# Performance work log

Hardware: AMD Instinct MI355X
Metric: run time of the kernel (lower is better)

## Reference

```python
import jax, jax.numpy as jnp
import numpy as np

NUM_HEADS = 8
NUM_LAYERS = 4
BASE_THR = 0.5     # AdaptiveLIF base_threshold (state reset -> no adaptation on single step)
TAU_MEM = 5.0      # tau_mem (single step from zero state: mem = decay*0 + x = x)
SURR_SLOPE = 5.0   # fast-sigmoid surrogate slope (forward path unaffected)
EPS = 1e-5
NEG = -1e9


@jax.custom_vjp
def spike(u):
    return (u > 0.0).astype(u.dtype)

def _spike_fwd(u):
    return (u > 0.0).astype(u.dtype), u

def _spike_bwd(u, g):
    return (g / (1.0 + SURR_SLOPE * jnp.abs(u)) ** 2,)

spike.defvjp(_spike_fwd, _spike_bwd)


def lif(x):
    # AdaptiveLIF, single timestep from reset state: mem = x, thr = base_threshold
    return spike(x - BASE_THR)


def layer_norm(x, g, b):
    m = jnp.mean(x, axis=-1, keepdims=True)
    v = jnp.mean((x - m) ** 2, axis=-1, keepdims=True)
    return (x - m) * jax.lax.rsqrt(v + EPS) * g + b


def dsa(x, wq, bq, wk, bk, wv, bv, wo, bo, top_k):
    # Dynamic Sparse Attention: dense scores -> per-query top-k mask -> softmax -> AV
    B, T, D = x.shape
    H = NUM_HEADS
    dh = D // H

    def heads(w, bias):
        return (x @ w.T + bias).reshape(B, T, H, dh).transpose(0, 2, 1, 3)  # [B,H,T,dh]

    q, k, v = heads(wq, bq), heads(wk, bk), heads(wv, bv)
    scores = jnp.einsum('bhqd,bhkd->bhqk', q, k) / jnp.sqrt(jnp.asarray(dh, x.dtype))
    vals, idx = jax.lax.top_k(scores, top_k)  # [B,H,T,K]

    # scatter top-k values into a -inf-filled score matrix (exact top-k sparsity)
    N = B * H * T
    rows = jnp.arange(N)[:, None]
    sp = jnp.full((N, T), NEG, scores.dtype).at[rows, idx.reshape(N, top_k)].set(vals.reshape(N, top_k))
    attn = jax.nn.softmax(sp.reshape(B, H, T, T), axis=-1)

    out = jnp.einsum('bhqk,bhkd->bhqd', attn, v)
    out = out.transpose(0, 2, 1, 3).reshape(B, T, D)
    out = out @ wo.T + bo
    return lif(out)  # spiking output of attention


def ffn(x, w1, b1, w2, b2):
    h = lif(x @ w1.T + b1)
    return lif(h @ w2.T + b2)


def setup_inputs() -> dict:
    key = jax.random.key(0)
    ks = jax.random.split(key, 16)
    L, D, F, IN, OUT, B, T = NUM_LAYERS, 512, 2048, 128, 256, 2, 2048
    s = 0.02
    return {
        'x': jax.random.normal(ks[0], (B, T, IN), jnp.float32),
        'emb_w': jax.random.normal(ks[1], (D, IN), jnp.float32) * s,
        'emb_b': jnp.zeros((D,), jnp.float32),
        'pos_emb': jax.random.normal(ks[2], (1, T, D), jnp.float32) * s,
        'wq': jax.random.normal(ks[3], (L, D, D), jnp.float32) * s,
        'bq': jnp.zeros((L, D), jnp.float32),
        'wk': jax.random.normal(ks[4], (L, D, D), jnp.float32) * s,
        'bk': jnp.zeros((L, D), jnp.float32),
        'wv': jax.random.normal(ks[5], (L, D, D), jnp.float32) * s,
        'bv': jnp.zeros((L, D), jnp.float32),
        'wo': jax.random.normal(ks[6], (L, D, D), jnp.float32) * s,
        'bo': jnp.zeros((L, D), jnp.float32),
        'ln1_g': jnp.ones((L, D), jnp.float32),
        'ln1_b': jnp.zeros((L, D), jnp.float32),
        'fc1_w': jax.random.normal(ks[7], (L, F, D), jnp.float32) * s,
        'fc1_b': jnp.zeros((L, F), jnp.float32),
        'fc2_w': jax.random.normal(ks[8], (L, D, F), jnp.float32) * s,
        'fc2_b': jnp.zeros((L, D), jnp.float32),
        'ln2_g': jnp.ones((L, D), jnp.float32),
        'ln2_b': jnp.zeros((L, D), jnp.float32),
        'fnorm_g': jnp.ones((D,), jnp.float32),
        'fnorm_b': jnp.zeros((D,), jnp.float32),
        'cls_w': jax.random.normal(ks[9], (OUT, D), jnp.float32) * s,
        'cls_b': jnp.zeros((OUT,), jnp.float32),
        'top_k': 32,
    }


def reference(x, emb_w, emb_b, pos_emb, wq, bq, wk, bk, wv, bv, wo, bo,
              ln1_g, ln1_b, fc1_w, fc1_b, fc2_w, fc2_b, ln2_g, ln2_b,
              fnorm_g, fnorm_b, cls_w, cls_b, top_k):
    B, T, _ = x.shape
    h = x @ emb_w.T + emb_b + pos_emb[:, :T, :]
    for l in range(NUM_LAYERS):
        a = dsa(h, wq[l], bq[l], wk[l], bk[l], wv[l], bv[l], wo[l], bo[l], top_k)
        h = layer_norm(h + a, ln1_g[l], ln1_b[l])
        f = ffn(h, fc1_w[l], fc1_b[l], fc2_w[l], fc2_b[l])
        h = layer_norm(h + f, ln2_g[l], ln2_b[l])
    h = layer_norm(h, fnorm_g, fnorm_b)
    pooled = jnp.mean(h, axis=1)  # [B, D]
    return pooled @ cls_w.T + cls_b
```

## Files before the change

kernel.cpp:

```cpp
#include <hip/hip_runtime.h>
#include <math.h>
#include <float.h>

#define T_SEQ  2048
#define DMODEL 512
#define NHEAD  8
#define DHEAD  64
#define FDIM   2048
#define NLAYER 4
#define NB     2
#define MROWS  (NB*T_SEQ)

typedef _Float16 f16x8 __attribute__((ext_vector_type(8)));
typedef float    f32x4 __attribute__((ext_vector_type(4)));

__device__ __forceinline__ void async16(const _Float16* g, _Float16* l) {
    __builtin_amdgcn_global_load_lds(
        (const __attribute__((address_space(1))) unsigned int*)g,
        (__attribute__((address_space(3))) unsigned int*)l, 16, 0, 0);
}

template<int BN, int EPI>
__global__ __launch_bounds__(256) void gemm_k(
    const float* __restrict__ A, const float* __restrict__ W,
    const float* __restrict__ bias, const float* __restrict__ pos,
    float* __restrict__ C, int M, int N, int K)
{
    constexpr int BM = 128;
    constexpr int BK = 32;
    constexpr int MN = BN / 16;
    __shared__ float As[BK][BM + 4];
    __shared__ float Ws[BK][BN + 4];
    const int tid = threadIdx.x;
    const int n0 = blockIdx.x * BN;
    const int m0 = blockIdx.y * BM;
    const int tx = tid & 15;
    const int ty = tid >> 4;

    float acc[8][MN];
    #pragma unroll
    for (int i = 0; i < 8; ++i)
        #pragma unroll
        for (int j = 0; j < MN; ++j) acc[i][j] = 0.f;

    for (int k0 = 0; k0 < K; k0 += BK) {
        #pragma unroll
        for (int it = 0; it < 4; ++it) {
            int qq = tid + 256 * it;
            int m = qq >> 3, kq = qq & 7;
            float4 v4 = *(const float4*)(A + (size_t)(m0 + m) * K + k0 + kq * 4);
            As[kq*4+0][m] = v4.x; As[kq*4+1][m] = v4.y;
            As[kq*4+2][m] = v4.z; As[kq*4+3][m] = v4.w;
        }
        #pragma unroll
        for (int it = 0; it < BN/32; ++it) {
            int qq = tid + 256 * it;
            int n = qq >> 3, kq = qq & 7;
            float4 v4 = *(const float4*)(W + (size_t)(n0 + n) * K + k0 + kq * 4);
            Ws[kq*4+0][n] = v4.x; Ws[kq*4+1][n] = v4.y;
            Ws[kq*4+2][n] = v4.z; Ws[kq*4+3][n] = v4.w;
        }
        __syncthreads();
        for (int kk = 0; kk < BK; ++kk) {
            float a[8], b[MN];
            float4 a0 = *(const float4*)&As[kk][ty*8];
            float4 a1 = *(const float4*)&As[kk][ty*8+4];
            a[0]=a0.x; a[1]=a0.y; a[2]=a0.z; a[3]=a0.w;
            a[4]=a1.x; a[5]=a1.y; a[6]=a1.z; a[7]=a1.w;
            float4 b0 = *(const float4*)&Ws[kk][tx*4];
            b[0]=b0.x; b[1]=b0.y; b[2]=b0.z; b[3]=b0.w;
            if constexpr (MN == 8) {
                float4 b1 = *(const float4*)&Ws[kk][64 + tx*4];
                b[4]=b1.x; b[5]=b1.y; b[6]=b1.z; b[7]=b1.w;
            }
            #pragma unroll
            for (int i = 0; i < 8; ++i)
                #pragma unroll
                for (int j = 0; j < MN; ++j)
                    acc[i][j] = fmaf(a[i], b[j], acc[i][j]);
        }
        __syncthreads();
    }

    #pragma unroll
    for (int i = 0; i < 8; ++i) {
        int m = m0 + ty*8 + i;
        #pragma unroll
        for (int jb = 0; jb < MN/4; ++jb) {
            int nn = n0 + jb*64 + tx*4;
            float4 r;
            r.x = acc[i][jb*4+0] + bias[nn+0];
            r.y = acc[i][jb*4+1] + bias[nn+1];
            r.z = acc[i][jb*4+2] + bias[nn+2];
            r.w = acc[i][jb*4+3] + bias[nn+3];
            if constexpr (EPI == 1) {
                const float* pp = pos + (size_t)(m & (T_SEQ-1)) * DMODEL + nn;
                r.x += pp[0]; r.y += pp[1]; r.z += pp[2]; r.w += pp[3];
            }
            *(float4*)(C + (size_t)m * N + nn) = r;
        }
    }
}

template<int BM, int BN, int ASRC, int EPI, int LAYOUT>
__global__ __launch_bounds__(256, (BM == 64) ? 3 : 2) void mgemm_k(
    const _Float16* __restrict__ AH, const _Float16* __restrict__ AL,
    const _Float16* __restrict__ WH, const _Float16* __restrict__ WL,
    const float* __restrict__ bias,
    float* __restrict__ O0, float* __restrict__ O1, float* __restrict__ O2,
    float* __restrict__ O3, float* __restrict__ O4,
    int M, int N, int K)
{
    constexpr int MI = BM / 32;
    constexpr int NJ = BN / 32;
    __shared__ _Float16 AsH[4][BM][8];
    __shared__ _Float16 AsL[(ASRC == 0) ? 4 : 1][BM][8];
    __shared__ _Float16 WsH[4][BN][8];
    __shared__ _Float16 WsL[4][BN][8];

    const int tid = threadIdx.x;
    const int n0 = blockIdx.x * BN;
    const int m0 = blockIdx.y * BM;
    const int wv = tid >> 6, lane = tid & 63;
    const int mw = (wv >> 1) * (BM/2), nw = (wv & 1) * (BN/2);
    const int fr = lane & 15;
    const int kb = lane >> 4;

    const int wsrow = tid >> 1;
    const int wskb  = (tid & 1) * 2;
    const int wkoff = (tid & 1) * 16;

    f32x4 acc[MI][NJ];
    #pragma unroll
    for (int i = 0; i < MI; ++i)
        #pragma unroll
        for (int j = 0; j < NJ; ++j) acc[i][j] = (f32x4)(0.f);

    for (int k0 = 0; k0 < K; k0 += 32) {
        if constexpr (BM == 128) {
            const _Float16* ap = AH + (size_t)(m0 + wsrow) * K + k0 + wkoff;
            *(f16x8*)&AsH[wskb  ][wsrow][0] = *(const f16x8*)ap;
            *(f16x8*)&AsH[wskb+1][wsrow][0] = *(const f16x8*)(ap + 8);
            if constexpr (ASRC == 0) {
                const _Float16* alp = AL + (size_t)(m0 + wsrow) * K + k0 + wkoff;
                *(f16x8*)&AsL[wskb  ][wsrow][0] = *(const f16x8*)alp;
                *(f16x8*)&AsL[wskb+1][wsrow][0] = *(const f16x8*)(alp + 8);
            }
        } else {
            const int arow = tid >> 2, akb = tid & 3;
            *(f16x8*)&AsH[akb][arow][0] =
                *(const f16x8*)(AH + (size_t)(m0 + arow) * K + k0 + akb*8);
            if constexpr (ASRC == 0)
                *(f16x8*)&AsL[akb][arow][0] =
                    *(const f16x8*)(AL + (size_t)(m0 + arow) * K + k0 + akb*8);
        }
        if constexpr (BN == 128) {
            const _Float16* wp = WH + (size_t)(n0 + wsrow) * K + k0 + wkoff;
            *(f16x8*)&WsH[wskb  ][wsrow][0] = *(const f16x8*)wp;
            *(f16x8*)&WsH[wskb+1][wsrow][0] = *(const f16x8*)(wp + 8);
            const _Float16* wlp = WL + (size_t)(n0 + wsrow) * K + k0 + wkoff;
            *(f16x8*)&WsL[wskb  ][wsrow][0] = *(const f16x8*)wlp;
            *(f16x8*)&WsL[wskb+1][wsrow][0] = *(const f16x8*)(wlp + 8);
        } else {
            const int wrow = tid >> 2, wwkb = tid & 3;
            *(f16x8*)&WsH[wwkb][wrow][0] =
                *(const f16x8*)(WH + (size_t)(n0 + wrow) * K + k0 + wwkb*8);
            *(f16x8*)&WsL[wwkb][wrow][0] =
                *(const f16x8*)(WL + (size_t)(n0 + wrow) * K + k0 + wwkb*8);
        }
        __syncthreads();

        f16x8 aH[MI], aL[MI], bH[NJ], bL[NJ];
        #pragma unroll
        for (int i = 0; i < MI; ++i) {
            aH[i] = *(const f16x8*)&AsH[kb][mw + i*16 + fr][0];
            if constexpr (ASRC == 0) aL[i] = *(const f16x8*)&AsL[kb][mw + i*16 + fr][0];
        }
        #pragma unroll
        for (int j = 0; j < NJ; ++j) {
            bH[j] = *(const f16x8*)&WsH[kb][nw + j*16 + fr][0];
            bL[j] = *(const f16x8*)&WsL[kb][nw + j*16 + fr][0];
        }
        #pragma unroll
        for (int i = 0; i < MI; ++i)
            #pragma unroll
            for (int j = 0; j < NJ; ++j) {
                acc[i][j] = __builtin_amdgcn_mfma_f32_16x16x32_f16(aH[i], bH[j], acc[i][j], 0, 0, 0);
                acc[i][j] = __builtin_amdgcn_mfma_f32_16x16x32_f16(aH[i], bL[j], acc[i][j], 0, 0, 0);
                if constexpr (ASRC == 0)
                    acc[i][j] = __builtin_amdgcn_mfma_f32_16x16x32_f16(aL[i], bH[j], acc[i][j], 0, 0, 0);
            }
        __syncthreads();
    }

    const int qq = lane >> 4;
    #pragma unroll
    for (int j = 0; j < NJ; ++j) {
        int n = n0 + nw + j*16 + fr;
        float bv = bias[n];
        #pragma unroll
        for (int i = 0; i < MI; ++i) {
            #pragma unroll
            for (int r = 0; r < 4; ++r) {
                int m = m0 + mw + i*16 + qq*4 + r;
                float val = acc[i][j][r] * (1.f/1024.f) + bv;
                if constexpr (EPI == 2) val = val > 0.5f ? 1.f : 0.f;
                if constexpr (EPI == 3) {
                    ((_Float16*)O0)[(size_t)m * N + n] = (val > 0.5f) ? (_Float16)16.f : (_Float16)0.f;
                } else if constexpr (LAYOUT == 0) {
                    O0[(size_t)m * N + n] = val;
                } else {
                    int b_ = m >> 11, t_ = m & (T_SEQ-1);
                    if (n < 512) {
                        size_t hl = (((size_t)(b_*NHEAD + (n>>6))*T_SEQ + t_) << 6) + (n & 63);
                        float s16 = 16.f * val;
                        _Float16 hh = (_Float16)s16;
                        ((_Float16*)O0)[hl] = hh;
                        ((_Float16*)O1)[hl] = (_Float16)(s16 - (float)hh);
                    } else if (n < 1024) {
                        int nn = n - 512;
                        size_t hl = (((size_t)(b_*NHEAD + (nn>>6))*T_SEQ + t_) << 6) + (nn & 63);
                        float s16 = 16.f * val;
                        _Float16 hh = (_Float16)s16;
                        ((_Float16*)O2)[hl] = hh;
                        ((_Float16*)O3)[hl] = (_Float16)(s16 - (float)hh);
                    } else {
                        int nn = n - 1024;
                        O4[(((size_t)(b_*NHEAD + (nn>>6))*T_SEQ + t_) << 6) + (nn & 63)] = val;
                    }
                }
            }
        }
    }
}

__global__ __launch_bounds__(256) void cvtw_k(
    const float* __restrict__ w, _Float16* __restrict__ H, _Float16* __restrict__ L,
    int n, float scale)
{
    int i = blockIdx.x * 256 + threadIdx.x;
    if (i < n) {
        float s = scale * w[i];
        _Float16 h = (_Float16)s;
        H[i] = h;
        L[i] = (_Float16)(s - (float)h);
    }
}

__global__ __launch_bounds__(256) void cvtlayer_k(
    const float* __restrict__ wq, const float* __restrict__ wk, const float* __restrict__ wv,
    const float* __restrict__ bq, const float* __restrict__ bk, const float* __restrict__ bv,
    const float* __restrict__ wo, const float* __restrict__ f1w, const float* __restrict__ f2w,
    _Float16* __restrict__ WcatH, _Float16* __restrict__ WcatL, float* __restrict__ bcat,
    _Float16* __restrict__ WoH, _Float16* __restrict__ WoL,
    _Float16* __restrict__ W1H, _Float16* __restrict__ W1L,
    _Float16* __restrict__ W2H, _Float16* __restrict__ W2L)
{
    int i = blockIdx.x * 256 + threadIdx.x;
    float w;
    _Float16 *H, *L;
    int off;
    if (i < 786432) {
        int src = i >> 18, o = i & 262143;
        w = (src == 0 ? wq : (src == 1 ? wk : wv))[o];
        H = WcatH; L = WcatL; off = i;
    } else if (i < 1048576) {
        off = i - 786432;  w = wo[off];  H = WoH; L = WoL;
    } else if (i < 2097152) {
        off = i - 1048576; w = f1w[off]; H = W1H; L = W1L;
    } else if (i < 3145728) {
        off = i - 2097152; w = f2w[off]; H = W2H; L = W2L;
    } else if (i < 3145728 + 1536) {
        int j = i - 3145728;
        int src = j >> 9, o = j & 511;
        bcat[j] = (src == 0 ? bq : (src == 1 ? bk : bv))[o];
        return;
    } else return;
    float s = 64.f * w;
    _Float16 h = (_Float16)s;
    H[off] = h;
    L[off] = (_Float16)(s - (float)h);
}

__global__ __launch_bounds__(512, 4) void attn_k(
    const _Float16* __restrict__ qH, const _Float16* __restrict__ qL,
    const _Float16* __restrict__ kH, const _Float16* __restrict__ kL,
    const float* __restrict__ v,
    _Float16* __restrict__ outH, _Float16* __restrict__ outL)
{
    __shared__ unsigned char lds[66560];
    _Float16* ksH = (_Float16*)(lds);
    _Float16* ksL = (_Float16*)(lds + 16384);
    float    (*ss)[132] = (float(*)[132])(lds + 32768);
    float*   wrow       = (float*)(lds + 32768);
    int*     irow       = (int*)(lds + 32768 + 8448);

    const int tid = threadIdx.x;
    const int bh  = blockIdx.y;
    const int t0  = blockIdx.x * 64;
    const _Float16* qHb = qH + ((size_t)bh * T_SEQ + t0) * DHEAD;
    const _Float16* qLb = qL + ((size_t)bh * T_SEQ + t0) * DHEAD;
    const _Float16* kHb = kH + (size_t)bh * T_SEQ * DHEAD;
    const _Float16* kLb = kL + (size_t)bh * T_SEQ * DHEAD;
    const float*    vb  = v  + (size_t)bh * T_SEQ * DHEAD;

    unsigned kreg[32];
    #pragma unroll
    for (int i = 0; i < 32; ++i) kreg[i] = 0u;

    const int wv = tid >> 6, lane = tid & 63;
    const int fr = lane & 15, q4 = lane >> 4;
    const int mh  = (wv >> 2) * 32;
    const int c0w = (wv & 3) * 32;
    const int srow = tid >> 3;
    const int ssub = tid & 7;

    f16x8 qaH[2][2], qaL[2][2];
    #pragma unroll
    for (int ks = 0; ks < 2; ++ks) {
        const int doff = ks*32 + q4*8;
        qaH[ks][0] = *(const f16x8*)(qHb + (mh + fr)*DHEAD + doff);
        qaH[ks][1] = *(const f16x8*)(qHb + (mh + 16 + fr)*DHEAD + doff);
        qaL[ks][0] = *(const f16x8*)(qLb + (mh + fr)*DHEAD + doff);
        qaL[ks][1] = *(const f16x8*)(qLb + (mh + 16 + fr)*DHEAD + doff);
    }

    auto stage = [&](int jt) {
        const int j0 = jt * 128;
        #pragma unroll
        for (int i = 0; i < 2; ++i) {
            const int r0 = wv*16 + i*8;
            const int cc = r0 + (lane >> 3);
            const int ch = (lane & 7) ^ (cc & 7);
            const size_t goff = (size_t)(j0 + cc) * DHEAD + ch*8;
            async16(kHb + goff, ksH + r0*64);
            async16(kLb + goff, ksL + r0*64);
        }
    };

    stage(0);
    __syncthreads();

    for (int jt = 0; jt < 16; ++jt) {
        const int j0 = jt * 128;

        f32x4 acc[2][2];
        acc[0][0] = (f32x4)(0.f); acc[0][1] = (f32x4)(0.f);
        acc[1][0] = (f32x4)(0.f); acc[1][1] = (f32x4)(0.f);
        #pragma unroll
        for (int ks = 0; ks < 2; ++ks) {
            const int chq  = ks*4 + q4;
            #pragma unroll
            for (int nj = 0; nj < 2; ++nj) {
                const int cc = c0w + nj*16 + fr;
                const int sl = cc*64 + (chq ^ (cc & 7))*8;
                f16x8 bHf = *(const f16x8*)&ksH[sl];
                f16x8 bLf = *(const f16x8*)&ksL[sl];
                acc[0][nj] = __builtin_amdgcn_mfma_f32_16x16x32_f16(qaH[ks][0], bHf, acc[0][nj], 0, 0, 0);
                acc[0][nj] = __builtin_amdgcn_mfma_f32_16x16x32_f16(qaH[ks][0], bLf, acc[0][nj], 0, 0, 0);
                acc[0][nj] = __builtin_amdgcn_mfma_f32_16x16x32_f16(qaL[ks][0], bHf, acc[0][nj], 0, 0, 0);
                acc[1][nj] = __builtin_amdgcn_mfma_f32_16x16x32_f16(qaH[ks][1], bHf, acc[1][nj], 0, 0, 0);
                acc[1][nj] = __builtin_amdgcn_mfma_f32_16x16x32_f16(qaH[ks][1], bLf, acc[1][nj], 0, 0, 0);
                acc[1][nj] = __builtin_amdgcn_mfma_f32_16x16x32_f16(qaL[ks][1], bHf, acc[1][nj], 0, 0, 0);
            }
        }
        #pragma unroll
        for (int mi = 0; mi < 2; ++mi)
            #pragma unroll
            for (int nj = 0; nj < 2; ++nj)
                #pragma unroll
                for (int r = 0; r < 4; ++r)
                    ss[mh + mi*16 + q4*4 + r][c0w + nj*16 + fr] = acc[mi][nj][r] * (1.f/2048.f);
        __syncthreads();

        if (jt < 15) stage(jt + 1);

        float4 c4[4];
        {
            const float* ssr = &ss[srow][0] + ssub*4;
            #pragma unroll
            for (int g = 0; g < 4; ++g) c4[g] = *(const float4*)(ssr + g*32);
        }
        unsigned cand[16];
        #pragma unroll
        for (int g = 0; g < 4; ++g) {
            float vg[4] = {c4[g].x, c4[g].y, c4[g].z, c4[g].w};
            #pragma unroll
            for (int r = 0; r < 4; ++r) {
                unsigned u = __float_as_uint(vg[r]);
                u ^= (unsigned)((int)u >> 31) | 0x80000000u;
                int col = ssub*4 + g*32 + r;
                cand[g*4+r] = (u & 0xFFFFF800u) | (unsigned)(2047 - (j0 + col));
            }
        }
        #pragma unroll
        for (int k2 = 2; k2 <= 16; k2 <<= 1) {
            #pragma unroll
            for (int j2 = k2 >> 1; j2 > 0; j2 >>= 1) {
                #pragma unroll
                for (int i2 = 0; i2 < 16; ++i2) {
                    int l2 = i2 ^ j2;
                    if (l2 > i2) {
                        unsigned a = cand[i2], b = cand[l2];
                        unsigned mn = a < b ? a : b;
                        unsigned mx = a < b ? b : a;
                        if ((i2 & k2) == 0) { cand[i2] = mx; cand[l2] = mn; }
                        else                { cand[i2] = mn; cand[l2] = mx; }
                    }
                }
            }
        }
        #pragma unroll
        for (int j2 = 0; j2 < 16; ++j2) {
            unsigned b = cand[15 - j2];
            if (kreg[16 + j2] < b) kreg[16 + j2] = b;
        }
        #pragma unroll
        for (int st = 16; st >= 1; st >>= 1) {
            #pragma unroll
            for (int i2 = 0; i2 < 32; ++i2) {
                if ((i2 & st) == 0) {
                    unsigned lo = kreg[i2], hi = kreg[i2 | st];
                    kreg[i2]      = lo < hi ? hi : lo;
                    kreg[i2 | st] = lo < hi ? lo : hi;
                }
            }
        }
        __syncthreads();
    }

    #pragma unroll
    for (int s = 1; s <= 4; s <<= 1) {
        #pragma unroll
        for (int i = 0; i < 16; ++i) {
            unsigned pa = (unsigned)__shfl_xor((int)kreg[31-i], s, 64);
            unsigned pb = (unsigned)__shfl_xor((int)kreg[i],    s, 64);
            if (pa > kreg[i])    kreg[i]    = pa;
            if (pb > kreg[31-i]) kreg[31-i] = pb;
        }
        #pragma unroll
        for (int st = 16; st >= 1; st >>= 1) {
            #pragma unroll
            for (int i2 = 0; i2 < 32; ++i2) {
                if ((i2 & st) == 0) {
                    unsigned lo = kreg[i2], hi = kreg[i2 | st];
                    kreg[i2]      = lo < hi ? hi : lo;
                    kreg[i2 | st] = lo < hi ? lo : hi;
                }
            }
        }
    }

    if (ssub == 0) {
        float w[32];
        #pragma unroll
        for (int i = 0; i < 32; ++i) {
            unsigned um = kreg[i] & 0xFFFFF800u;
            unsigned ub = (um & 0x80000000u) ? (um ^ 0x80000000u) : ~um;
            w[i] = __uint_as_float(ub);
        }
        float m = w[0];
        float s = 0.f;
        #pragma unroll
        for (int i = 0; i < 32; ++i) { w[i] = __expf(w[i] - m); s += w[i]; }
        float inv = 1.f / s;
        #pragma unroll
        for (int i = 0; i < 32; ++i) {
            wrow[srow*33 + i] = w[i] * inv;
            irow[srow*33 + i] = 2047 - (int)(kreg[i] & 0x7FFu);
        }
    }
    __syncthreads();

    const int wid = tid >> 6, lane2 = tid & 63;
    const int b = bh >> 3, h = bh & 7;
    for (int rr = wid; rr < 64; rr += 8) {
        float a0 = 0.f, a1 = 0.f, a2 = 0.f, a3 = 0.f;
        #pragma unroll
        for (int i = 0; i < 8; ++i) {
            a0 = fmaf(wrow[rr*33 + i],      vb[(size_t)irow[rr*33 + i]      * DHEAD + lane2], a0);
            a1 = fmaf(wrow[rr*33 + 8 + i],  vb[(size_t)irow[rr*33 + 8 + i]  * DHEAD + lane2], a1);
            a2 = fmaf(wrow[rr*33 + 16 + i], vb[(size_t)irow[rr*33 + 16 + i] * DHEAD + lane2], a2);
            a3 = fmaf(wrow[rr*33 + 24 + i], vb[(size_t)irow[rr*33 + 24 + i] * DHEAD + lane2], a3);
        }
        float accv = (a0 + a1) + (a2 + a3);
        size_t oi = ((size_t)(b * T_SEQ + t0 + rr)) * DMODEL + h * DHEAD + lane2;
        float s16 = 16.f * accv;
        _Float16 hh = (_Float16)s16;
        outH[oi] = hh;
        outL[oi] = (_Float16)(s16 - (float)hh);
    }
}

__global__ __launch_bounds__(256) void ln_k(
    const float* __restrict__ x, const float* __restrict__ res,
    const float* __restrict__ g, const float* __restrict__ bb,
    float* __restrict__ out, _Float16* __restrict__ oH, _Float16* __restrict__ oL)
{
    __shared__ float red[8];
    const int row = blockIdx.x;
    const int tid = threadIdx.x;
    const float* xr = x + (size_t)row * DMODEL;
    float v0 = xr[tid], v1 = xr[tid + 256];
    if (res) {
        const float* rr = res + (size_t)row * DMODEL;
        v0 += rr[tid]; v1 += rr[tid + 256];
    }
    float s = v0 + v1;
    #pragma unroll
    for (int o = 1; o < 64; o <<= 1) s += __shfl_xor(s, o);
    const int wid = tid >> 6, lane = tid & 63;
    if (lane == 0) red[wid] = s;
    __syncthreads();
    float mean = (red[0] + red[1] + red[2] + red[3]) * (1.f / DMODEL);
    float d0 = v0 - mean, d1 = v1 - mean;
    float qs = d0*d0 + d1*d1;
    #pragma unroll
    for (int o = 1; o < 64; o <<= 1) qs += __shfl_xor(qs, o);
    if (lane == 0) red[4 + wid] = qs;
    __syncthreads();
    float var = (red[4] + red[5] + red[6] + red[7]) * (1.f / DMODEL);
    float rs = rsqrtf(var + 1e-5f);
    float o0 = d0 * rs * g[tid]       + bb[tid];
    float o1 = d1 * rs * g[tid + 256] + bb[tid + 256];
    size_t base = (size_t)row * DMODEL;
    out[base + tid]       = o0;
    out[base + tid + 256] = o1;
    float s0 = 16.f * o0, s1 = 16.f * o1;
    _Float16 h0 = (_Float16)s0, h1 = (_Float16)s1;
    oH[base + tid]       = h0;
    oH[base + tid + 256] = h1;
    oL[base + tid]       = (_Float16)(s0 - (float)h0);
    oL[base + tid + 256] = (_Float16)(s1 - (float)h1);
}

__global__ __launch_bounds__(256) void pool_k(
    const float* __restrict__ h, float* __restrict__ part)
{
    const int chunk = blockIdx.x & 15;
    const int idx = (blockIdx.x >> 4) * 256 + threadIdx.x;
    const int b = idx >> 9, d = idx & 511;
    const float* p = h + ((size_t)b * T_SEQ + chunk * 128) * DMODEL + d;
    float s = 0.f;
    for (int t = 0; t < 128; ++t) s += p[(size_t)t * DMODEL];
    part[chunk * 1024 + idx] = s;
}

__global__ __launch_bounds__(256) void poolsum_k(
    const float* __restrict__ part, float* __restrict__ pooled)
{
    int idx = blockIdx.x * 256 + threadIdx.x;
    float s = 0.f;
    #pragma unroll
    for (int c = 0; c < 16; ++c) s += part[c * 1024 + idx];
    pooled[idx] = s * (1.f / T_SEQ);
}

__global__ __launch_bounds__(256) void cls_k(
    const float* __restrict__ pooled, const float* __restrict__ w,
    const float* __restrict__ bias, float* __restrict__ out)
{
    const int wid = threadIdx.x >> 6, lane = threadIdx.x & 63;
    const int oi = blockIdx.x * 4 + wid;
    const int b = oi >> 8, o = oi & 255;
    const float* pr = pooled + b * DMODEL;
    const float* wr = w + (size_t)o * DMODEL;
    float s = 0.f;
    for (int d = lane; d < DMODEL; d += 64) s = fmaf(pr[d], wr[d], s);
    #pragma unroll
    for (int off = 1; off < 64; off <<= 1) s += __shfl_xor(s, off);
    if (lane == 0) out[oi] = s + bias[o];
}

extern "C" void kernel_launch(void* const* d_in, const int* in_sizes, int n_in,
                              void* d_out, int out_size, void* d_ws, size_t ws_size,
                              hipStream_t stream)
{
    const float* x     = (const float*)d_in[0];
    const float* emb_w = (const float*)d_in[1];
    const float* emb_b = (const float*)d_in[2];
    const float* pos   = (const float*)d_in[3];
    const float* wq    = (const float*)d_in[4];
    const float* bq    = (const float*)d_in[5];
    const float* wk    = (const float*)d_in[6];
    const float* bk    = (const float*)d_in[7];
    const float* wv    = (const float*)d_in[8];
    const float* bv    = (const float*)d_in[9];
    const float* wo    = (const float*)d_in[10];
    const float* bo    = (const float*)d_in[11];
    const float* ln1g  = (const float*)d_in[12];
    const float* ln1b  = (const float*)d_in[13];
    const float* fc1w  = (const float*)d_in[14];
    const float* fc1b  = (const float*)d_in[15];
    const float* fc2w  = (const float*)d_in[16];
    const float* fc2b  = (const float*)d_in[17];
    const float* ln2g  = (const float*)d_in[18];
    const float* ln2b  = (const float*)d_in[19];
    const float* fng   = (const float*)d_in[20];
    const float* fnb   = (const float*)d_in[21];
    const float* clsw  = (const float*)d_in[22];
    const float* clsb  = (const float*)d_in[23];

    float* ws = (float*)d_ws;
    const size_t SZ  = (size_t)MROWS * DMODEL;
    const size_t HP  = SZ / 2;
    float*     h     = ws;
    float*     t1    = ws + 1*SZ;
    _Float16*  hH    = (_Float16*)(ws + 2*SZ);
    _Float16*  hL    = (_Float16*)(ws + 2*SZ + HP);
    _Float16*  aoH   = (_Float16*)(ws + 3*SZ);
    _Float16*  aoL   = (_Float16*)(ws + 3*SZ + HP);
    _Float16*  qbH   = (_Float16*)(ws + 4*SZ);
    _Float16*  qbL   = (_Float16*)(ws + 4*SZ + HP);
    _Float16*  kbH   = (_Float16*)(ws + 5*SZ);
    _Float16*  kbL   = (_Float16*)(ws + 5*SZ + HP);
    float*     vbuf  = ws + 6*SZ;
    _Float16*  WcatH = (_Float16*)(ws + 7*SZ);
    _Float16*  WcatL = (_Float16*)(ws + 7*SZ + 393216);
    _Float16*  WoH   = (_Float16*)(ws + 7*SZ + 786432);
    _Float16*  WoL   = (_Float16*)(ws + 7*SZ + 917504);
    _Float16*  W1H   = (_Float16*)(ws + 7*SZ + 1048576);
    _Float16*  W1L   = (_Float16*)(ws + 7*SZ + 1572864);
    _Float16*  W2H   = (_Float16*)(ws + 7*SZ + 2097152);
    _Float16*  W2L   = (_Float16*)(ws + 7*SZ + 2621440);
    float*     bcat  = ws + 7*SZ + 3145728;
    float*     pooled= ws + 7*SZ + 3145728 + 1536;
    float*     part  = ws + 7*SZ + 3145728 + 1536 + 1024;
    _Float16*  hid   = (_Float16*)(ws + 4*SZ);
    const size_t needed = (7*SZ + 3145728 + 1536 + 1024 + 16384) * sizeof(float);
    if (ws_size < needed) return;

    dim3 blk(256);

    gemm_k<64,1><<<dim3(DMODEL/64, MROWS/128), blk, 0, stream>>>(
        x, emb_w, emb_b, pos, h, MROWS, DMODEL, 128);
    cvtw_k<<<dim3((int)(SZ/256)), blk, 0, stream>>>(h, hH, hL, (int)SZ, 16.f);

    for (int l = 0; l < NLAYER; ++l) {
        const float* wq_l = wq + (size_t)l*DMODEL*DMODEL;
        const float* bq_l = bq + (size_t)l*DMODEL;
        const float* wk_l = wk + (size_t)l*DMODEL*DMODEL;
        const float* bk_l = bk + (size_t)l*DMODEL;
        const float* wv_l = wv + (size_t)l*DMODEL*DMODEL;
        const float* bv_l = bv + (size_t)l*DMODEL;
        const float* wo_l = wo + (size_t)l*DMODEL*DMODEL;
        const float* bo_l = bo + (size_t)l*DMODEL;
        const float* f1w_l = fc1w + (size_t)l*FDIM*DMODEL;
        const float* f1b_l = fc1b + (size_t)l*FDIM;
        const float* f2w_l = fc2w + (size_t)l*DMODEL*FDIM;
        const float* f2b_l = fc2b + (size_t)l*DMODEL;

        cvtlayer_k<<<dim3(12294), blk, 0, stream>>>(
            wq_l, wk_l, wv_l, bq_l, bk_l, bv_l, wo_l, f1w_l, f2w_l,
            WcatH, WcatL, bcat, WoH, WoL, W1H, W1L, W2H, W2L);

        mgemm_k<64,128,0,0,2><<<dim3(12, 64), blk, 0, stream>>>(
            hH, hL, WcatH, WcatL, bcat,
            (float*)qbH, (float*)qbL, (float*)kbH, (float*)kbL, vbuf,
            MROWS, 1536, DMODEL);

        attn_k<<<dim3(T_SEQ/64, NB*NHEAD), dim3(512), 0, stream>>>(
            qbH, qbL, kbH, kbL, vbuf, aoH, aoL);

        mgemm_k<64,64,0,2,0><<<dim3(8, 64), blk, 0, stream>>>(
            aoH, aoL, WoH, WoL, bo_l, t1, nullptr, nullptr, nullptr, nullptr,
            MROWS, DMODEL, DMODEL);
        ln_k<<<dim3(MROWS), blk, 0, stream>>>(h, t1, ln1g + (size_t)l*DMODEL,
                                              ln1b + (size_t)l*DMODEL, h, hH, hL);

        mgemm_k<128,128,0,3,0><<<dim3(16, 32), blk, 0, stream>>>(
            hH, hL, W1H, W1L, f1b_l, (float*)hid, nullptr, nullptr, nullptr, nullptr,
            MROWS, FDIM, DMODEL);
        mgemm_k<64,64,1,2,0><<<dim3(8, 64), blk, 0, stream>>>(
            hid, nullptr, W2H, W2L, f2b_l, t1, nullptr, nullptr, nullptr, nullptr,
            MROWS, DMODEL, FDIM);
        ln_k<<<dim3(MROWS), blk, 0, stream>>>(h, t1, ln2g + (size_t)l*DMODEL,
                                              ln2b + (size_t)l*DMODEL, h, hH, hL);
    }

    ln_k<<<dim3(MROWS), blk, 0, stream>>>(h, nullptr, fng, fnb, h, hH, hL);
    pool_k<<<dim3(64), blk, 0, stream>>>(h, part);
    poolsum_k<<<dim3(4), blk, 0, stream>>>(part, pooled);
    cls_k<<<dim3(128), blk, 0, stream>>>(pooled, clsw, clsb, (float*)d_out);
}
```

Measured before the change: 1.152 ms.

## Double-buffer LDS tiles in split-fp16 MFMA GEMM with register prefetch

The split-fp16 MFMA GEMM kernel now keeps two LDS buffers per operand and prefetches the next K-slice from global memory into registers while the current slice is computed. The registers are written to the other buffer afterwards, which removes one __syncthreads per iteration and hides global load latency behind the MFMA work. In exchange it doubles LDS use and adds prefetch registers, which may lower occupancy under the existing launch bounds.

```diff
diff --git a/kernel.cpp b/kernel.cpp
--- a/kernel.cpp
+++ b/kernel.cpp
@@ -113,10 +113,10 @@
 {
     constexpr int MI = BM / 32;
     constexpr int NJ = BN / 32;
-    __shared__ _Float16 AsH[4][BM][8];
-    __shared__ _Float16 AsL[(ASRC == 0) ? 4 : 1][BM][8];
-    __shared__ _Float16 WsH[4][BN][8];
-    __shared__ _Float16 WsL[4][BN][8];
+    __shared__ _Float16 AsH[2][4][BM][8];
+    __shared__ _Float16 AsL[(ASRC == 0) ? 2 : 1][(ASRC == 0) ? 4 : 1][(ASRC == 0) ? BM : 1][8];
+    __shared__ _Float16 WsH[2][4][BN][8];
+    __shared__ _Float16 WsL[2][4][BN][8];
 
     const int tid = threadIdx.x;
     const int n0 = blockIdx.x * BN;
@@ -129,57 +129,87 @@
     const int wsrow = tid >> 1;
     const int wskb  = (tid & 1) * 2;
     const int wkoff = (tid & 1) * 16;
-
-    f32x4 acc[MI][NJ];
-    #pragma unroll
-    for (int i = 0; i < MI; ++i)
-        #pragma unroll
-        for (int j = 0; j < NJ; ++j) acc[i][j] = (f32x4)(0.f);
-
-    for (int k0 = 0; k0 < K; k0 += 32) {
+    const int arow  = tid >> 2, akb = tid & 3;
+
+    f16x8 pa0, pa1, pal0, pal1, pw0, pw1, pwl0, pwl1;
+
+    auto gload = [&](int k0) {
         if constexpr (BM == 128) {
             const _Float16* ap = AH + (size_t)(m0 + wsrow) * K + k0 + wkoff;
-            *(f16x8*)&AsH[wskb  ][wsrow][0] = *(const f16x8*)ap;
-            *(f16x8*)&AsH[wskb+1][wsrow][0] = *(const f16x8*)(ap + 8);
+            pa0 = *(const f16x8*)ap;
+            pa1 = *(const f16x8*)(ap + 8);
             if constexpr (ASRC == 0) {
                 const _Float16* alp = AL + (size_t)(m0 + wsrow) * K + k0 + wkoff;
-                *(f16x8*)&AsL[wskb  ][wsrow][0] = *(const f16x8*)alp;
-                *(f16x8*)&AsL[wskb+1][wsrow][0] = *(const f16x8*)(alp + 8);
+                pal0 = *(const f16x8*)alp;
+                pal1 = *(const f16x8*)(alp + 8);
             }
         } else {
-            const int arow = tid >> 2, akb = tid & 3;
-            *(f16x8*)&AsH[akb][arow][0] =
-                *(const f16x8*)(AH + (size_t)(m0 + arow) * K + k0 + akb*8);
+            pa0 = *(const f16x8*)(AH + (size_t)(m0 + arow) * K + k0 + akb*8);
             if constexpr (ASRC == 0)
-                *(f16x8*)&AsL[akb][arow][0] =
-                    *(const f16x8*)(AL + (size_t)(m0 + arow) * K + k0 + akb*8);
+                pal0 = *(const f16x8*)(AL + (size_t)(m0 + arow) * K + k0 + akb*8);
         }
         if constexpr (BN == 128) {
             const _Float16* wp = WH + (size_t)(n0 + wsrow) * K + k0 + wkoff;
-            *(f16x8*)&WsH[wskb  ][wsrow][0] = *(const f16x8*)wp;
-            *(f16x8*)&WsH[wskb+1][wsrow][0] = *(const f16x8*)(wp + 8);
+            pw0 = *(const f16x8*)wp;
+            pw1 = *(const f16x8*)(wp + 8);
             const _Float16* wlp = WL + (size_t)(n0 + wsrow) * K + k0 + wkoff;
-            *(f16x8*)&WsL[wskb  ][wsrow][0] = *(const f16x8*)wlp;
-            *(f16x8*)&WsL[wskb+1][wsrow][0] = *(const f16x8*)(wlp + 8);
+            pwl0 = *(const f16x8*)wlp;
+            pwl1 = *(const f16x8*)(wlp + 8);
         } else {
-            const int wrow = tid >> 2, wwkb = tid & 3;
-            *(f16x8*)&WsH[wwkb][wrow][0] =
-                *(const f16x8*)(WH + (size_t)(n0 + wrow) * K + k0 + wwkb*8);
-            *(f16x8*)&WsL[wwkb][wrow][0] =
-                *(const f16x8*)(WL + (size_t)(n0 + wrow) * K + k0 + wwkb*8);
-        }
-        __syncthreads();
+            pw0  = *(const f16x8*)(WH + (size_t)(n0 + arow) * K + k0 + akb*8);
+            pwl0 = *(const f16x8*)(WL + (size_t)(n0 + arow) * K + k0 + akb*8);
+        }
+    };
+    auto swrite = [&](int buf) {
+        if constexpr (BM == 128) {
+            *(f16x8*)&AsH[buf][wskb  ][wsrow][0] = pa0;
+            *(f16x8*)&AsH[buf][wskb+1][wsrow][0] = pa1;
+            if constexpr (ASRC == 0) {
+                *(f16x8*)&AsL[buf][wskb  ][wsrow][0] = pal0;
+                *(f16x8*)&AsL[buf][wskb+1][wsrow][0] = pal1;
+            }
+        } else {
+            *(f16x8*)&AsH[buf][akb][arow][0] = pa0;
+            if constexpr (ASRC == 0)
+                *(f16x8*)&AsL[buf][akb][arow][0] = pal0;
+        }
+        if constexpr (BN == 128) {
+            *(f16x8*)&WsH[buf][wskb  ][wsrow][0] = pw0;
+            *(f16x8*)&WsH[buf][wskb+1][wsrow][0] = pw1;
+            *(f16x8*)&WsL[buf][wskb  ][wsrow][0] = pwl0;
+            *(f16x8*)&WsL[buf][wskb+1][wsrow][0] = pwl1;
+        } else {
+            *(f16x8*)&WsH[buf][akb][arow][0] = pw0;
+            *(f16x8*)&WsL[buf][akb][arow][0] = pwl0;
+        }
+    };
+
+    f32x4 acc[MI][NJ];
+    #pragma unroll
+    for (int i = 0; i < MI; ++i)
+        #pragma unroll
+        for (int j = 0; j < NJ; ++j) acc[i][j] = (f32x4)(0.f);
+
+    const int NT = K >> 5;
+    int cur = 0;
+    gload(0);
+    swrite(0);
+    __syncthreads();
+
+    for (int t = 0; t < NT; ++t) {
+        const bool more = (t + 1 < NT);
+        if (more) gload((t + 1) << 5);
 
         f16x8 aH[MI], aL[MI], bH[NJ], bL[NJ];
         #pragma unroll
         for (int i = 0; i < MI; ++i) {
-            aH[i] = *(const f16x8*)&AsH[kb][mw + i*16 + fr][0];
-            if constexpr (ASRC == 0) aL[i] = *(const f16x8*)&AsL[kb][mw + i*16 + fr][0];
+            aH[i] = *(const f16x8*)&AsH[cur][kb][mw + i*16 + fr][0];
+            if constexpr (ASRC == 0) aL[i] = *(const f16x8*)&AsL[cur][kb][mw + i*16 + fr][0];
         }
         #pragma unroll
         for (int j = 0; j < NJ; ++j) {
-            bH[j] = *(const f16x8*)&WsH[kb][nw + j*16 + fr][0];
-            bL[j] = *(const f16x8*)&WsL[kb][nw + j*16 + fr][0];
+            bH[j] = *(const f16x8*)&WsH[cur][kb][nw + j*16 + fr][0];
+            bL[j] = *(const f16x8*)&WsL[cur][kb][nw + j*16 + fr][0];
         }
         #pragma unroll
         for (int i = 0; i < MI; ++i)
@@ -190,7 +220,11 @@
                 if constexpr (ASRC == 0)
                     acc[i][j] = __builtin_amdgcn_mfma_f32_16x16x32_f16(aL[i], bH[j], acc[i][j], 0, 0, 0);
             }
-        __syncthreads();
+        if (more) {
+            swrite(cur ^ 1);
+            __syncthreads();
+            cur ^= 1;
+        }
     }
 
     const int qq = lane >> 4;
```

After: 1.133 ms. No clear change (-1.6%).
